# Optimization experiments

Measured on AMD Instinct MI355X. Metric: run time of the kernel, lower is better.

## Reference

```python
import jax, jax.numpy as jnp
import numpy as np

TOP_K = 2  # top_k from __init__


def upfeat(x, prob, up_h=4, up_w=4):
    # x: [b,1,h,w], prob: [b,9,h*up_h,w*up_w]
    b, c, h, w = x.shape
    xp = jnp.pad(x, ((0, 0), (0, 0), (1, 1), (1, 1)))
    # 3x3 unfold with padding 1; torch F.unfold channel order is (dy, dx) row-major
    patches = jnp.stack([xp[:, 0, dy:dy + h, dx:dx + w]
                         for dy in range(3) for dx in range(3)], axis=1)  # [b,9,h,w]
    # nearest-neighbor upsample by integer factor == repeat along each spatial axis
    up = jnp.repeat(jnp.repeat(patches, up_h, axis=2), up_w, axis=3)  # [b,9,H,W]
    return jnp.sum(up * prob, axis=1, keepdims=True)  # [b,1,H,W]


def reference(cost, spg):
    # cost: [b,1,D,h,w], spg: [b,9,4h,4w]
    c = jnp.moveaxis(cost, 2, -1)  # [b,1,h,w,D]
    vals, inds = jax.lax.top_k(c, TOP_K)            # top-k over disparity
    corr = jax.nn.softmax(vals, axis=-1)            # [b,1,h,w,k]
    disp4 = jnp.sum(corr * inds.astype(cost.dtype), axis=-1)  # soft-argmax -> [b,1,h,w]
    disp1 = upfeat(disp4, spg, 4, 4)[:, 0] * 4.0    # [b,4h,4w]
    return disp1


def setup_inputs() -> dict:
    key = jax.random.key(0)
    k1, k2 = jax.random.split(key)
    cost = jax.random.normal(k1, (4, 1, 48, 128, 240), dtype=jnp.float32)
    spg = jax.random.uniform(k2, (4, 9, 512, 960), dtype=jnp.float32)
    return {"cost": cost, "spg": spg}
```

## Files before the change

### kernel.cpp

```cpp
#include <hip/hip_runtime.h>

#define B  4
#define D  48
#define H  128
#define W  240
#define H4 512
#define W4 960

__global__ void __launch_bounds__(256)
topk_softargmax_kernel(const float* __restrict__ cost, float* __restrict__ disp4) {
    int idx = blockIdx.x * blockDim.x + threadIdx.x;
    const int npix = B * H * W;
    if (idx >= npix) return;
    int b   = idx / (H * W);
    int rem = idx - b * (H * W);
    const float* p = cost + (size_t)b * D * H * W + rem;

    float v[D];
    #pragma unroll
    for (int d = 0; d < D; ++d) v[d] = p[(size_t)d * (H * W)];

    float v1 = -INFINITY, v2 = -INFINITY;
    int   i1 = 0,          i2 = 0;
    #pragma unroll
    for (int d = 0; d < D; ++d) {
        float x = v[d];
        if (x > v1)      { v2 = v1; i2 = i1; v1 = x; i1 = d; }
        else if (x > v2) { v2 = x;  i2 = d; }
    }
    float e     = expf(v2 - v1);
    float inv   = 1.0f / (1.0f + e);
    disp4[idx]  = ((float)i1 + (float)i2 * e) * inv;
}

__global__ void __launch_bounds__(256)
upfeat_kernel(const float* __restrict__ disp4, const float* __restrict__ spg,
              float* __restrict__ out) {
    int t = blockIdx.x * blockDim.x + threadIdx.x;
    const int nt = B * H4 * W;
    if (t >= nt) return;

    int xs  = t % W;
    int tmp = t / W;
    int Y   = tmp % H4;
    int b   = tmp / H4;
    int y   = Y >> 2;

    float dv[9];
    const float* dp = disp4 + (size_t)b * (H * W);
    #pragma unroll
    for (int dy = 0; dy < 3; ++dy) {
        int yy = y + dy - 1;
        #pragma unroll
        for (int dx = 0; dx < 3; ++dx) {
            int xx = xs + dx - 1;
            dv[dy * 3 + dx] = (yy >= 0 && yy < H && xx >= 0 && xx < W)
                              ? dp[yy * W + xx] : 0.0f;
        }
    }

    const float* sp = spg + (((size_t)b * 9) * H4 + Y) * W4 + 4 * xs;
    float4 acc = make_float4(0.f, 0.f, 0.f, 0.f);
    #pragma unroll
    for (int k = 0; k < 9; ++k) {
        float4 s = *reinterpret_cast<const float4*>(sp + (size_t)k * (H4 * W4));
        float  d = dv[k];
        acc.x += d * s.x; acc.y += d * s.y; acc.z += d * s.z; acc.w += d * s.w;
    }
    acc.x *= 4.f; acc.y *= 4.f; acc.z *= 4.f; acc.w *= 4.f;

    *reinterpret_cast<float4*>(out + ((size_t)b * H4 + Y) * W4 + 4 * xs) = acc;
}

extern "C" void kernel_launch(void* const* d_in, const int* in_sizes, int n_in,
                              void* d_out, int out_size, void* d_ws, size_t ws_size,
                              hipStream_t stream) {
    const float* cost = (const float*)d_in[0];
    const float* spg  = (const float*)d_in[1];
    float* outp  = (float*)d_out;
    float* disp4 = (float*)d_ws;

    {
        const int n = B * H * W;
        topk_softargmax_kernel<<<(n + 255) / 256, 256, 0, stream>>>(cost, disp4);
    }
    {
        const int n = B * H4 * W;
        upfeat_kernel<<<(n + 255) / 256, 256, 0, stream>>>(disp4, spg, outp);
    }
}
```

Before: 24.76 us.

## Fuse top-k soft-argmax and upfeat into one tiled kernel with shared-memory halo

Merges the two kernels into one. Each block computes soft-argmax disparities for a 16x16 tile plus a one-pixel halo into shared memory, then does the 3x3 weighted upsampling, with each thread writing 4 output rows. This removes the intermediate disparity buffer round trip and one kernel launch. In exchange, halo pixels are recomputed by neighbouring blocks and the 324-pixel tile is processed unevenly by 256 threads. The grid shrinks to 480 blocks, which limits latency hiding, and the cost-load and spg-load phases are serialized within each block.

```diff
diff --git a/kernel.cpp b/kernel.cpp
--- a/kernel.cpp
+++ b/kernel.cpp
@@ -6,70 +6,76 @@
 #define W  240
 #define H4 512
 #define W4 960
+#define TS 16
 
 __global__ void __launch_bounds__(256)
-topk_softargmax_kernel(const float* __restrict__ cost, float* __restrict__ disp4) {
-    int idx = blockIdx.x * blockDim.x + threadIdx.x;
-    const int npix = B * H * W;
-    if (idx >= npix) return;
-    int b   = idx / (H * W);
-    int rem = idx - b * (H * W);
-    const float* p = cost + (size_t)b * D * H * W + rem;
+fused_disp_upfeat_kernel(const float* __restrict__ cost,
+                         const float* __restrict__ spg,
+                         float* __restrict__ out) {
+    __shared__ float sd[TS + 2][TS + 3];
 
-    float v[D];
-    #pragma unroll
-    for (int d = 0; d < D; ++d) v[d] = p[(size_t)d * (H * W)];
+    int blk = blockIdx.x;
+    int txt = blk % (W / TS);
+    int rem = blk / (W / TS);
+    int tyt = rem % (H / TS);
+    int b   = rem / (H / TS);
+    int x0  = txt * TS - 1;
+    int y0  = tyt * TS - 1;
 
-    float v1 = -INFINITY, v2 = -INFINITY;
-    int   i1 = 0,          i2 = 0;
-    #pragma unroll
-    for (int d = 0; d < D; ++d) {
-        float x = v[d];
-        if (x > v1)      { v2 = v1; i2 = i1; v1 = x; i1 = d; }
-        else if (x > v2) { v2 = x;  i2 = d; }
+    for (int i = threadIdx.x; i < (TS + 2) * (TS + 2); i += 256) {
+        int iy = i / (TS + 2);
+        int ix = i - iy * (TS + 2);
+        int y  = y0 + iy;
+        int x  = x0 + ix;
+        float dres = 0.0f;
+        if ((unsigned)x < W && (unsigned)y < H) {
+            const float* p = cost + (size_t)b * (D * H * W) + y * W + x;
+            float v[D];
+            #pragma unroll
+            for (int d = 0; d < D; ++d) v[d] = p[(size_t)d * (H * W)];
+            float v1 = -INFINITY, v2 = -INFINITY;
+            int   i1 = 0,          i2 = 0;
+            #pragma unroll
+            for (int d = 0; d < D; ++d) {
+                float xv = v[d];
+                if (xv > v1)      { v2 = v1; i2 = i1; v1 = xv; i1 = d; }
+                else if (xv > v2) { v2 = xv; i2 = d; }
+            }
+            float e = expf(v2 - v1);
+            dres = ((float)i1 + (float)i2 * e) / (1.0f + e);
+        }
+        sd[iy][ix] = dres;
     }
-    float e     = expf(v2 - v1);
-    float inv   = 1.0f / (1.0f + e);
-    disp4[idx]  = ((float)i1 + (float)i2 * e) * inv;
-}
+    __syncthreads();
 
-__global__ void __launch_bounds__(256)
-upfeat_kernel(const float* __restrict__ disp4, const float* __restrict__ spg,
-              float* __restrict__ out) {
-    int t = blockIdx.x * blockDim.x + threadIdx.x;
-    const int nt = B * H4 * W;
-    if (t >= nt) return;
-
-    int xs  = t % W;
-    int tmp = t / W;
-    int Y   = tmp % H4;
-    int b   = tmp / H4;
-    int y   = Y >> 2;
+    int t  = threadIdx.x;
+    int cx = t & (TS - 1);
+    int cy = t >> 4;
 
     float dv[9];
-    const float* dp = disp4 + (size_t)b * (H * W);
     #pragma unroll
-    for (int dy = 0; dy < 3; ++dy) {
-        int yy = y + dy - 1;
+    for (int dy = 0; dy < 3; ++dy)
         #pragma unroll
-        for (int dx = 0; dx < 3; ++dx) {
-            int xx = xs + dx - 1;
-            dv[dy * 3 + dx] = (yy >= 0 && yy < H && xx >= 0 && xx < W)
-                              ? dp[yy * W + xx] : 0.0f;
+        for (int dx = 0; dx < 3; ++dx)
+            dv[dy * 3 + dx] = sd[cy + dy][cx + dx];
+
+    int xs  = x0 + 1 + cx;
+    int Yb  = (y0 + 1 + cy) * 4;
+
+    #pragma unroll
+    for (int r = 0; r < 4; ++r) {
+        int Y = Yb + r;
+        const float* sp = spg + ((size_t)(b * 9) * H4 + Y) * W4 + xs * 4;
+        float4 acc = make_float4(0.f, 0.f, 0.f, 0.f);
+        #pragma unroll
+        for (int k = 0; k < 9; ++k) {
+            float4 s = *reinterpret_cast<const float4*>(sp + (size_t)k * (H4 * W4));
+            float  d = dv[k];
+            acc.x += d * s.x; acc.y += d * s.y; acc.z += d * s.z; acc.w += d * s.w;
         }
+        acc.x *= 4.f; acc.y *= 4.f; acc.z *= 4.f; acc.w *= 4.f;
+        *reinterpret_cast<float4*>(out + ((size_t)b * H4 + Y) * W4 + xs * 4) = acc;
     }
-
-    const float* sp = spg + (((size_t)b * 9) * H4 + Y) * W4 + 4 * xs;
-    float4 acc = make_float4(0.f, 0.f, 0.f, 0.f);
-    #pragma unroll
-    for (int k = 0; k < 9; ++k) {
-        float4 s = *reinterpret_cast<const float4*>(sp + (size_t)k * (H4 * W4));
-        float  d = dv[k];
-        acc.x += d * s.x; acc.y += d * s.y; acc.z += d * s.z; acc.w += d * s.w;
-    }
-    acc.x *= 4.f; acc.y *= 4.f; acc.z *= 4.f; acc.w *= 4.f;
-
-    *reinterpret_cast<float4*>(out + ((size_t)b * H4 + Y) * W4 + 4 * xs) = acc;
 }
 
 extern "C" void kernel_launch(void* const* d_in, const int* in_sizes, int n_in,
@@ -77,15 +83,8 @@
                               hipStream_t stream) {
     const float* cost = (const float*)d_in[0];
     const float* spg  = (const float*)d_in[1];
-    float* outp  = (float*)d_out;
-    float* disp4 = (float*)d_ws;
+    float* outp = (float*)d_out;
 
-    {
-        const int n = B * H * W;
-        topk_softargmax_kernel<<<(n + 255) / 256, 256, 0, stream>>>(cost, disp4);
-    }
-    {
-        const int n = B * H4 * W;
-        upfeat_kernel<<<(n + 255) / 256, 256, 0, stream>>>(disp4, spg, outp);
-    }
+    const int nblk = (W / TS) * (H / TS) * B;
+    fused_disp_upfeat_kernel<<<nblk, 256, 0, stream>>>(cost, spg, outp);
 }
```

Result: slower. 30.89 us (+24.7%).

## Split top-k disparity scan across lanes and tile upsampling with shared halo

Applied to the files above, without the earlier changes.

The top-k kernel now has four lanes work on four adjacent pixels together. Each lane reads a quarter of the disparity range with float4 loads, and the partial top-2 results are merged with xor shuffles that keep lower-index tie-breaking. The upsample kernel now works in 16x8 coarse tiles. Each block stages the disparity halo in shared memory, so the 3x3 neighbourhood no longer needs repeated global gathers. In exchange, upsampling has shorter contiguous row segments per block and extra synchronisation, while the main cost remains the bandwidth-bound streaming of spg.

```diff
diff --git a/kernel.cpp b/kernel.cpp
--- a/kernel.cpp
+++ b/kernel.cpp
@@ -1,75 +1,132 @@
 #include <hip/hip_runtime.h>
 
-#define B  4
-#define D  48
-#define H  128
-#define W  240
-#define H4 512
-#define W4 960
+#define B   4
+#define D   48
+#define H   128
+#define W   240
+#define H4  512
+#define W4  960
+#define HW  (H * W)
+#define NPIX (B * HW)
+#define DQ  (D / 4)
 
 __global__ void __launch_bounds__(256)
 topk_softargmax_kernel(const float* __restrict__ cost, float* __restrict__ disp4) {
-    int idx = blockIdx.x * blockDim.x + threadIdx.x;
-    const int npix = B * H * W;
-    if (idx >= npix) return;
-    int b   = idx / (H * W);
-    int rem = idx - b * (H * W);
-    const float* p = cost + (size_t)b * D * H * W + rem;
+    int gid  = blockIdx.x * 256 + threadIdx.x;
+    int q    = gid & 3;
+    int pix0 = (gid >> 2) * 4;
+    int b    = pix0 / HW;
+    int rem  = pix0 - b * HW;
+    const float* p = cost + (size_t)b * (D * HW) + (size_t)(q * DQ) * HW + rem;
 
-    float v[D];
+    float4 vv[DQ];
     #pragma unroll
-    for (int d = 0; d < D; ++d) v[d] = p[(size_t)d * (H * W)];
+    for (int j = 0; j < DQ; ++j)
+        vv[j] = *reinterpret_cast<const float4*>(p + (size_t)j * HW);
 
-    float v1 = -INFINITY, v2 = -INFINITY;
-    int   i1 = 0,          i2 = 0;
+    float v1[4], v2[4]; int i1[4], i2[4];
     #pragma unroll
-    for (int d = 0; d < D; ++d) {
-        float x = v[d];
-        if (x > v1)      { v2 = v1; i2 = i1; v1 = x; i1 = d; }
-        else if (x > v2) { v2 = x;  i2 = d; }
-    }
-    float e     = expf(v2 - v1);
-    float inv   = 1.0f / (1.0f + e);
-    disp4[idx]  = ((float)i1 + (float)i2 * e) * inv;
-}
+    for (int c = 0; c < 4; ++c) { v1[c] = -INFINITY; v2[c] = -INFINITY; i1[c] = 0; i2[c] = 0; }
 
-__global__ void __launch_bounds__(256)
-upfeat_kernel(const float* __restrict__ disp4, const float* __restrict__ spg,
-              float* __restrict__ out) {
-    int t = blockIdx.x * blockDim.x + threadIdx.x;
-    const int nt = B * H4 * W;
-    if (t >= nt) return;
-
-    int xs  = t % W;
-    int tmp = t / W;
-    int Y   = tmp % H4;
-    int b   = tmp / H4;
-    int y   = Y >> 2;
-
-    float dv[9];
-    const float* dp = disp4 + (size_t)b * (H * W);
     #pragma unroll
-    for (int dy = 0; dy < 3; ++dy) {
-        int yy = y + dy - 1;
+    for (int j = 0; j < DQ; ++j) {
+        int d = q * DQ + j;
+        float xs[4] = { vv[j].x, vv[j].y, vv[j].z, vv[j].w };
         #pragma unroll
-        for (int dx = 0; dx < 3; ++dx) {
-            int xx = xs + dx - 1;
-            dv[dy * 3 + dx] = (yy >= 0 && yy < H && xx >= 0 && xx < W)
-                              ? dp[yy * W + xx] : 0.0f;
+        for (int c = 0; c < 4; ++c) {
+            float x = xs[c];
+            if (x > v1[c])      { v2[c] = v1[c]; i2[c] = i1[c]; v1[c] = x; i1[c] = d; }
+            else if (x > v2[c]) { v2[c] = x;  i2[c] = d; }
         }
     }
 
-    const float* sp = spg + (((size_t)b * 9) * H4 + Y) * W4 + 4 * xs;
-    float4 acc = make_float4(0.f, 0.f, 0.f, 0.f);
     #pragma unroll
-    for (int k = 0; k < 9; ++k) {
-        float4 s = *reinterpret_cast<const float4*>(sp + (size_t)k * (H4 * W4));
-        float  d = dv[k];
-        acc.x += d * s.x; acc.y += d * s.y; acc.z += d * s.z; acc.w += d * s.w;
+    for (int step = 1; step <= 2; step <<= 1) {
+        bool lower = (q & step) == 0;
+        #pragma unroll
+        for (int c = 0; c < 4; ++c) {
+            float pv1 = __shfl_xor(v1[c], step);
+            int   pi1 = __shfl_xor(i1[c], step);
+            float pv2 = __shfl_xor(v2[c], step);
+            int   pi2 = __shfl_xor(i2[c], step);
+            float av1, av2, bv1, bv2; int ai1, ai2, bi1, bi2;
+            if (lower) { av1=v1[c]; ai1=i1[c]; av2=v2[c]; ai2=i2[c]; bv1=pv1; bi1=pi1; bv2=pv2; bi2=pi2; }
+            else       { av1=pv1;   ai1=pi1;   av2=pv2;   ai2=pi2;   bv1=v1[c]; bi1=i1[c]; bv2=v2[c]; bi2=i2[c]; }
+            if (bv1 > av1) {
+                v1[c] = bv1; i1[c] = bi1;
+                if (av1 >= bv2) { v2[c] = av1; i2[c] = ai1; } else { v2[c] = bv2; i2[c] = bi2; }
+            } else {
+                v1[c] = av1; i1[c] = ai1;
+                if (av2 >= bv1) { v2[c] = av2; i2[c] = ai2; } else { v2[c] = bv1; i2[c] = bi1; }
+            }
+        }
     }
-    acc.x *= 4.f; acc.y *= 4.f; acc.z *= 4.f; acc.w *= 4.f;
 
-    *reinterpret_cast<float4*>(out + ((size_t)b * H4 + Y) * W4 + 4 * xs) = acc;
+    if (q == 0) {
+        float4 r;
+        { float e = expf(v2[0]-v1[0]); r.x = ((float)i1[0] + (float)i2[0]*e) / (1.0f+e); }
+        { float e = expf(v2[1]-v1[1]); r.y = ((float)i1[1] + (float)i2[1]*e) / (1.0f+e); }
+        { float e = expf(v2[2]-v1[2]); r.z = ((float)i1[2] + (float)i2[2]*e) / (1.0f+e); }
+        { float e = expf(v2[3]-v1[3]); r.w = ((float)i1[3] + (float)i2[3]*e) / (1.0f+e); }
+        *reinterpret_cast<float4*>(disp4 + pix0) = r;
+    }
+}
+
+#define TSX 16
+#define TSY 8
+__global__ void __launch_bounds__(256)
+upfeat_tile_kernel(const float* __restrict__ disp4, const float* __restrict__ spg,
+                   float* __restrict__ out) {
+    __shared__ float sd[TSY + 2][TSX + 3];
+
+    int blk = blockIdx.x;
+    int txt = blk % (W / TSX);
+    int rem = blk / (W / TSX);
+    int tyt = rem % (H / TSY);
+    int b   = rem / (H / TSY);
+    int x0  = txt * TSX;
+    int y0  = tyt * TSY;
+
+    int i = threadIdx.x;
+    if (i < (TSY + 2) * (TSX + 2)) {
+        int hy = i / (TSX + 2);
+        int hx = i - hy * (TSX + 2);
+        int y  = y0 + hy - 1;
+        int x  = x0 + hx - 1;
+        float v = 0.0f;
+        if ((unsigned)y < H && (unsigned)x < W)
+            v = disp4[(size_t)b * HW + y * W + x];
+        sd[hy][hx] = v;
+    }
+    __syncthreads();
+
+    int fx4 = threadIdx.x & (TSX - 1);
+    int fyb = threadIdx.x >> 4;
+
+    #pragma unroll
+    for (int rep = 0; rep < 2; ++rep) {
+        int fy = fyb + rep * 16;
+        int cy = fy >> 2;
+        float dv[9];
+        #pragma unroll
+        for (int dy = 0; dy < 3; ++dy)
+            #pragma unroll
+            for (int dx = 0; dx < 3; ++dx)
+                dv[dy * 3 + dx] = sd[cy + dy][fx4 + dx];
+
+        int Y  = y0 * 4 + fy;
+        int X4 = x0 + fx4;
+        const float* sp = spg + ((size_t)(b * 9) * H4 + Y) * W4 + X4 * 4;
+        float4 acc = make_float4(0.f, 0.f, 0.f, 0.f);
+        #pragma unroll
+        for (int k = 0; k < 9; ++k) {
+            float4 s = *reinterpret_cast<const float4*>(sp + (size_t)k * (H4 * W4));
+            float  d = dv[k];
+            acc.x += d * s.x; acc.y += d * s.y; acc.z += d * s.z; acc.w += d * s.w;
+        }
+        acc.x *= 4.f; acc.y *= 4.f; acc.z *= 4.f; acc.w *= 4.f;
+        *reinterpret_cast<float4*>(out + ((size_t)b * H4 + Y) * W4 + X4 * 4) = acc;
+    }
 }
 
 extern "C" void kernel_launch(void* const* d_in, const int* in_sizes, int n_in,
@@ -81,11 +138,11 @@
     float* disp4 = (float*)d_ws;
 
     {
-        const int n = B * H * W;
+        const int n = NPIX;
         topk_softargmax_kernel<<<(n + 255) / 256, 256, 0, stream>>>(cost, disp4);
     }
     {
-        const int n = B * H4 * W;
-        upfeat_kernel<<<(n + 255) / 256, 256, 0, stream>>>(disp4, spg, outp);
+        const int nblk = (W / TSX) * (H / TSY) * B;
+        upfeat_tile_kernel<<<nblk, 256, 0, stream>>>(disp4, spg, outp);
     }
 }
```

Result: slower. 26.10 us (+5.4%).
